# Kernel tuning notes

Measured on AMD Instinct MI355X. Metric: run time of the kernel, lower is better.

The kernel has to match this reference:

```python
import jax, jax.numpy as jnp
import numpy as np

TEMPERATURE = 5.0

def setup_inputs() -> dict:
    key = jax.random.key(0)
    k1, k2 = jax.random.split(key)
    B, D = 8192, 128
    features = jax.random.normal(k1, (B, D), dtype=jnp.float32)
    labels = jax.random.randint(k2, (B,), 0, 100, dtype=jnp.int64)
    return {"features": features, "labels": labels, "fac_label": 3}


def reference(features, labels, fac_label):
    # features: [B, D], labels: [B]
    B = features.shape[0]
    # positive-pair mask; note original's mask_scale row-copy loop is a no-op,
    # so mask_scale == mask, and mask_cross_feature == ones (fac_label unused in effect)
    mask = (labels[:, None] == labels[None, :]).astype(features.dtype)  # [B, B]

    sim = jnp.matmul(features, features.T) / TEMPERATURE  # [B, B]
    logits_max = jax.lax.stop_gradient(jnp.max(sim, axis=1, keepdims=True))
    logits = sim - logits_max

    # remove self-contrast (diagonal)
    logits_mask = 1.0 - jnp.eye(B, dtype=features.dtype)
    mask = mask * logits_mask

    exp_logits = jnp.exp(logits) * logits_mask
    log_prob = logits - jnp.log(1e-12 + exp_logits.sum(axis=1, keepdims=True))

    mean_log_prob_pos_mask = (mask * log_prob).sum(axis=1)  # [B]
    # vectorized form of the per-element reciprocal loop: 1/count where count>0 else 0
    cnt = mask.sum(axis=1)
    recip = jnp.where(cnt == 0, 0.0, 1.0 / jnp.where(cnt == 0, 1.0, cnt))

    loss = -(mean_log_prob_pos_mask * recip).mean()
    return loss
```

## Files before the change

### kernel.cpp

```cpp
#include <hip/hip_runtime.h>


#define BN 8192
#define DK 128
#define INV_T 0.2f
#define C1F 0.28853901f
#define C40F 27.7258872f

#define CHUNKS 32
#define CCOLS (BN / CHUNKS)
#define RPB 256
#define RT 4
#define NJT (CCOLS / 16)

#define NCLS 100
#define PB 128
#define PROWS (BN / PB)

#define OFF_FB    0
#define OFF_PART  (2 * 1024 * 1024)
#define OFF_GP    (OFF_PART + 2 * 1024 * 1024)
#define OFF_HISTP (OFF_GP + PB * NCLS * DK * 4)
#define OFF_G     (OFF_HISTP + PB * NCLS * 4)
#define OFF_HIST  (OFF_G + NCLS * DK * 4)
#define OFF_BSUM  (OFF_HIST + 512)
#define OFF_CTR   (OFF_BSUM + 256)

typedef __attribute__((ext_vector_type(8))) short bf16x8;
typedef __attribute__((ext_vector_type(4))) float f32x4;

__device__ __forceinline__ unsigned short f2bf(float f) {
    unsigned u = __builtin_bit_cast(unsigned, f);
    u += 0x7fffu + ((u >> 16) & 1u);
    return (unsigned short)(u >> 16);
}

__device__ __forceinline__ float fexp2(float x) {
#if __has_builtin(__builtin_amdgcn_exp2f)
    return __builtin_amdgcn_exp2f(x);
#else
    float r; asm("v_exp_f32 %0, %1" : "=v"(r) : "v"(x)); return r;
#endif
}

__device__ __forceinline__ void load_lds16(const void* g, void* l) {
    __builtin_amdgcn_global_load_lds(
        (const __attribute__((address_space(1))) unsigned int*)g,
        (__attribute__((address_space(3))) unsigned int*)l, 16, 0, 0);
}

__global__ __launch_bounds__(256) void prep_kernel(const float* __restrict__ F,
                                                   const int* __restrict__ labels,
                                                   unsigned short* __restrict__ Fb,
                                                   float* __restrict__ Gp,
                                                   int* __restrict__ histp,
                                                   unsigned int* __restrict__ ctr) {
    const int t  = threadIdx.x;
    const int b  = blockIdx.x;
    const int r0 = b * PROWS;

    if (b == 0 && t == 0) *ctr = 0u;

    const float4* F4  = (const float4*)F + (size_t)b * (PROWS * DK / 4);
    ushort4*      Fb4 = (ushort4*)Fb + (size_t)b * (PROWS * DK / 4);
#pragma unroll
    for (int k = 0; k < PROWS * DK / 4 / 256; ++k) {
        float4 v = F4[k * 256 + t];
        ushort4 o;
        o.x = f2bf(v.x); o.y = f2bf(v.y); o.z = f2bf(v.z); o.w = f2bf(v.w);
        Fb4[k * 256 + t] = o;
    }

    __shared__ int   lh[NCLS];
    __shared__ float gl[NCLS][DK];
    float* glf = (float*)gl;
    if (t < NCLS) lh[t] = 0;
#pragma unroll
    for (int k = 0; k < NCLS * DK / 256; ++k) glf[k * 256 + t] = 0.f;
    __syncthreads();

    if (t < PROWS) atomicAdd(&lh[labels[r0 + t]], 1);

    if (t < DK) {
        for (int rr = 0; rr < PROWS; ++rr) {
            const int row = r0 + rr;
            const int c   = labels[row];
            gl[c][t] += F[(size_t)row * DK + t];
        }
    }
    __syncthreads();

    if (t < NCLS) histp[b * NCLS + t] = lh[t];
#pragma unroll
    for (int k = 0; k < NCLS * DK / 256; ++k) {
        const int idx = k * 256 + t;
        Gp[(size_t)b * (NCLS * DK) + idx] = glf[idx];
    }
}

template <bool DIAGBLK>
__device__ __forceinline__ void supcon_rows(const short* __restrict__ Fb,
                                            float2* __restrict__ part,
                                            int bx, int by, char* smem) {
    const int t    = threadIdx.x;
    const int wave = t >> 6, lane = t & 63;
    const int quad = lane >> 4, l16 = lane & 15;
    const int rowBase = bx * RPB + wave * (RT * 16);
    const int colBase = by * CCOLS;

    bf16x8 a[RT][4];
#pragma unroll
    for (int rt = 0; rt < RT; ++rt)
#pragma unroll
        for (int kt = 0; kt < 4; ++kt)
            a[rt][kt] = *(const bf16x8*)(Fb + (size_t)(rowBase + rt * 16 + l16) * DK
                                            + kt * 32 + quad * 8);

    float mr[RT][4], Zs[RT][4];
#pragma unroll
    for (int rt = 0; rt < RT; ++rt)
#pragma unroll
        for (int r = 0; r < 4; ++r) { mr[rt][r] = -__builtin_inff(); Zs[rt][r] = 0.f; }

    const int  L    = wave * 1024 + lane * 16;
    const int  sw   = (L & ~255) | ((L & 255) ^ ((L >> 4) & 0x70));
    const char* tile0 = (const char*)(Fb + (size_t)colBase * DK);
    char*       dst0  = smem + wave * 1024;

    int roff[4];
#pragma unroll
    for (int kt = 0; kt < 4; ++kt)
        roff[kt] = l16 * 256 + ((kt * 64 + quad * 16) ^ ((l16 & 7) << 4));

    auto STAGE = [&](int bufoff, int jt) {
        load_lds16(tile0 + (size_t)jt * 4096 + sw, dst0 + bufoff);
    };

    auto COMPUTE = [&](int bufoff, int jt) {
        bf16x8 bb[4];
#pragma unroll
        for (int kt = 0; kt < 4; ++kt)
            bb[kt] = *(const bf16x8*)(smem + bufoff + roff[kt]);
        const int j0 = colBase + jt * 16;
#pragma unroll
        for (int rt = 0; rt < RT; ++rt) {
            f32x4 acc = {0.f, 0.f, 0.f, 0.f};
#pragma unroll
            for (int kt = 0; kt < 4; ++kt)
                acc = __builtin_amdgcn_mfma_f32_16x16x32_bf16(a[rt][kt], bb[kt], acc, 0, 0, 0);
#pragma unroll
            for (int r = 0; r < 4; ++r) {
                const float raw = acc[r];
                mr[rt][r] = fmaxf(mr[rt][r], raw);
                float e = fexp2(fmaf(raw, C1F, -40.0f));
                if (DIAGBLK) {
                    const int irow0 = rowBase + rt * 16 + quad * 4;
                    if (j0 + l16 == irow0 + r) e = 0.f;
                }
                Zs[rt][r] += e;
            }
        }
    };

    STAGE(0, 0);
    __syncthreads();
    for (int jt = 0; jt < NJT; jt += 2) {
        STAGE(4096, jt + 1);
        COMPUTE(0, jt);
        __syncthreads();
        if (jt + 2 < NJT) STAGE(0, jt + 2);
        COMPUTE(4096, jt + 1);
        __syncthreads();
    }

#pragma unroll
    for (int rt = 0; rt < RT; ++rt)
#pragma unroll
        for (int r = 0; r < 4; ++r) {
            float mm = mr[rt][r], zz = Zs[rt][r];
#pragma unroll
            for (int h = 1; h < 16; h <<= 1) {
                mm = fmaxf(mm, __shfl_xor(mm, h));
                zz += __shfl_xor(zz, h);
            }
            if (l16 == 0)
                part[(size_t)by * BN + rowBase + rt * 16 + quad * 4 + r] =
                    make_float2(mm, zz);
        }
}

__global__ __launch_bounds__(256) void supcon_main(const short* __restrict__ Fb,
                                                   float2* __restrict__ part,
                                                   const float* __restrict__ Gp,
                                                   const int* __restrict__ histp,
                                                   float* __restrict__ G,
                                                   int* __restrict__ hist) {
    __shared__ alignas(16) char smem[8192];
    if (blockIdx.y == CHUNKS) {
        const int base = blockIdx.x * 256 + threadIdx.x;
        for (int idx = base; idx < NCLS * DK + NCLS; idx += BN) {
            if (idx < NCLS * DK) {
                float s = 0.f;
#pragma unroll 8
                for (int p = 0; p < PB; ++p) s += Gp[(size_t)p * (NCLS * DK) + idx];
                G[idx] = s;
            } else {
                const int c = idx - NCLS * DK;
                int s = 0;
#pragma unroll 8
                for (int p = 0; p < PB; ++p) s += histp[p * NCLS + c];
                hist[c] = s;
            }
        }
        return;
    }
    if (blockIdx.x == blockIdx.y) supcon_rows<true >(Fb, part, blockIdx.x, blockIdx.y, smem);
    else                          supcon_rows<false>(Fb, part, blockIdx.x, blockIdx.y, smem);
}

__global__ __launch_bounds__(256) void supcon_finalize(const float* __restrict__ F,
                                                       const int* __restrict__ labels,
                                                       const float2* __restrict__ part,
                                                       const float* __restrict__ G,
                                                       const int* __restrict__ hist,
                                                       float* __restrict__ bsums,
                                                       unsigned int* __restrict__ ctr,
                                                       float* __restrict__ out) {
    const int t = threadIdx.x;
    const int i = blockIdx.x * 256 + t;

    float mraw = -__builtin_inff(), Zm = 0.f;
#pragma unroll 8
    for (int c = 0; c < CHUNKS; ++c) {
        const float2 p = part[(size_t)c * BN + i];
        mraw = fmaxf(mraw, p.x);
        Zm += p.y;
    }
    const int   lbl = labels[i];
    const float cnt = (float)(hist[lbl] - 1);

    const float4* fr = (const float4*)(F + (size_t)i * DK);
    const float4* gr = (const float4*)(G + lbl * DK);
    float dot = 0.f, nrm = 0.f;
#pragma unroll 8
    for (int k = 0; k < DK / 4; ++k) {
        const float4 av = fr[k], gv = gr[k];
        dot += av.x * gv.x + av.y * gv.y + av.z * gv.z + av.w * gv.w;
        nrm += av.x * av.x + av.y * av.y + av.z * av.z + av.w * av.w;
    }

    const float m = mraw * INV_T;
    const float A = (dot - nrm) * INV_T;
    float term = 0.f;
    if (cnt > 0.5f)
        term = (A - cnt * m) / cnt - __logf(1e-12f + Zm * __expf(C40F - m));

    float sum = term;
#pragma unroll
    for (int h = 1; h < 64; h <<= 1) sum += __shfl_xor(sum, h);
    __shared__ float ss[4];
    if ((t & 63) == 0) ss[t >> 6] = sum;
    __syncthreads();
    if (t == 0) {
        bsums[blockIdx.x] = ss[0] + ss[1] + ss[2] + ss[3];
        __threadfence();
        const unsigned old = atomicAdd(ctr, 1u);
        if (old == (BN / 256) - 1) {
            __threadfence();
            float tot = 0.f;
            const volatile float* vb = bsums;
            for (int c = 0; c < BN / 256; ++c) tot += vb[c];
            out[0] = -tot * (1.0f / BN);
        }
    }
}

extern "C" void kernel_launch(void* const* d_in, const int* in_sizes, int n_in,
                              void* d_out, int out_size, void* d_ws, size_t ws_size,
                              hipStream_t stream) {
    const float* F      = (const float*)d_in[0];
    const int*   labels = (const int*)d_in[1];
    float* out = (float*)d_out;
    char*  ws  = (char*)d_ws;

    unsigned short* Fb    = (unsigned short*)(ws + OFF_FB);
    float2*         part  = (float2*)(ws + OFF_PART);
    float*          Gp    = (float*)(ws + OFF_GP);
    int*            histp = (int*)(ws + OFF_HISTP);
    float*          G     = (float*)(ws + OFF_G);
    int*            hist  = (int*)(ws + OFF_HIST);
    float*          bsums = (float*)(ws + OFF_BSUM);
    unsigned int*   ctr   = (unsigned int*)(ws + OFF_CTR);

    prep_kernel<<<PB, 256, 0, stream>>>(F, labels, Fb, Gp, histp, ctr);
    supcon_main<<<dim3(BN / RPB, CHUNKS + 1), 256, 0, stream>>>((const short*)Fb, part,
                                                                Gp, histp, G, hist);
    supcon_finalize<<<BN / 256, 256, 0, stream>>>(F, labels, part, G, hist,
                                                  bsums, ctr, out);
}
```

Before: 116.7 us.

## Deepen LDS staging to a four-buffer pipeline and parallelize class-sum prep

The main supcon loop moves from a double buffer to a four-slot LDS ring. Three tiles are prefetched ahead, and explicit vmcnt waits plus raw s_barrier calls replace __syncthreads, so global-to-LDS loads can overlap more MFMA work. The prep kernel now caches labels in LDS and uses all 256 threads, with two half-row groups accumulating into separate class-sum buffers that are summed on output. In exchange, LDS use doubles in both kernels, which may reduce occupancy, and the hand-written waitcnt and barrier sequencing has to stay correct.

Result: slower. 121.9 us (+4.4%).

```diff
diff --git a/kernel.cpp b/kernel.cpp
--- a/kernel.cpp
+++ b/kernel.cpp
@@ -28,6 +28,8 @@
 
 typedef __attribute__((ext_vector_type(8))) short bf16x8;
 typedef __attribute__((ext_vector_type(4))) float f32x4;
+
+#define FENCE() asm volatile("" ::: "memory")
 
 __device__ __forceinline__ unsigned short f2bf(float f) {
     unsigned u = __builtin_bit_cast(unsigned, f);
@@ -71,30 +73,35 @@
         Fb4[k * 256 + t] = o;
     }
 
+    __shared__ int   ll[PROWS];
     __shared__ int   lh[NCLS];
-    __shared__ float gl[NCLS][DK];
-    float* glf = (float*)gl;
+    __shared__ float gl[2][NCLS][DK];
+    float4* gl4 = (float4*)gl;
     if (t < NCLS) lh[t] = 0;
-#pragma unroll
-    for (int k = 0; k < NCLS * DK / 256; ++k) glf[k * 256 + t] = 0.f;
+    if (t < PROWS) ll[t] = labels[r0 + t];
+#pragma unroll
+    for (int k = 0; k < 2 * NCLS * DK / 4 / 256; ++k)
+        gl4[k * 256 + t] = make_float4(0.f, 0.f, 0.f, 0.f);
     __syncthreads();
 
-    if (t < PROWS) atomicAdd(&lh[labels[r0 + t]], 1);
-
-    if (t < DK) {
-        for (int rr = 0; rr < PROWS; ++rr) {
-            const int row = r0 + rr;
-            const int c   = labels[row];
-            gl[c][t] += F[(size_t)row * DK + t];
+    if (t < PROWS) atomicAdd(&lh[ll[t]], 1);
+
+    {
+        const int half = t >> 7, col = t & 127;
+        const int rb   = half * (PROWS / 2);
+        for (int rr = 0; rr < PROWS / 2; ++rr) {
+            const int lr = rb + rr;
+            gl[half][ll[lr]][col] += F[(size_t)(r0 + lr) * DK + col];
         }
     }
     __syncthreads();
 
     if (t < NCLS) histp[b * NCLS + t] = lh[t];
+    const float* gl0 = (const float*)gl;
 #pragma unroll
     for (int k = 0; k < NCLS * DK / 256; ++k) {
         const int idx = k * 256 + t;
-        Gp[(size_t)b * (NCLS * DK) + idx] = glf[idx];
+        Gp[(size_t)b * (NCLS * DK) + idx] = gl0[idx] + gl0[NCLS * DK + idx];
     }
 }
 
@@ -132,15 +139,15 @@
     for (int kt = 0; kt < 4; ++kt)
         roff[kt] = l16 * 256 + ((kt * 64 + quad * 16) ^ ((l16 & 7) << 4));
 
-    auto STAGE = [&](int bufoff, int jt) {
-        load_lds16(tile0 + (size_t)jt * 4096 + sw, dst0 + bufoff);
+    auto STAGE = [&](int buf, int jt) {
+        load_lds16(tile0 + (size_t)jt * 4096 + sw, dst0 + buf * 4096);
     };
 
-    auto COMPUTE = [&](int bufoff, int jt) {
+    auto COMPUTE = [&](int buf, int jt) {
         bf16x8 bb[4];
 #pragma unroll
         for (int kt = 0; kt < 4; ++kt)
-            bb[kt] = *(const bf16x8*)(smem + bufoff + roff[kt]);
+            bb[kt] = *(const bf16x8*)(smem + buf * 4096 + roff[kt]);
         const int j0 = colBase + jt * 16;
 #pragma unroll
         for (int rt = 0; rt < RT; ++rt) {
@@ -162,16 +169,27 @@
         }
     };
 
-    STAGE(0, 0);
-    __syncthreads();
-    for (int jt = 0; jt < NJT; jt += 2) {
-        STAGE(4096, jt + 1);
-        COMPUTE(0, jt);
-        __syncthreads();
-        if (jt + 2 < NJT) STAGE(0, jt + 2);
-        COMPUTE(4096, jt + 1);
-        __syncthreads();
-    }
+    STAGE(0, 0); STAGE(1, 1); STAGE(2, 2);
+    int jt = 0;
+    for (; jt < NJT - 2; ++jt) {
+        asm volatile("s_waitcnt vmcnt(2)" ::: "memory");
+        __builtin_amdgcn_s_barrier();
+        FENCE();
+        COMPUTE(jt & 3, jt);
+        FENCE();
+        __builtin_amdgcn_s_barrier();
+        FENCE();
+        if (jt + 3 < NJT) STAGE((jt + 3) & 3, jt + 3);
+    }
+    asm volatile("s_waitcnt vmcnt(1)" ::: "memory");
+    __builtin_amdgcn_s_barrier();
+    FENCE();
+    COMPUTE(jt & 3, jt);
+    ++jt;
+    asm volatile("s_waitcnt vmcnt(0)" ::: "memory");
+    __builtin_amdgcn_s_barrier();
+    FENCE();
+    COMPUTE(jt & 3, jt);
 
 #pragma unroll
     for (int rt = 0; rt < RT; ++rt)
@@ -195,7 +213,7 @@
                                                    const int* __restrict__ histp,
                                                    float* __restrict__ G,
                                                    int* __restrict__ hist) {
-    __shared__ alignas(16) char smem[8192];
+    __shared__ alignas(16) char smem[16384];
     if (blockIdx.y == CHUNKS) {
         const int base = blockIdx.x * 256 + threadIdx.x;
         for (int idx = base; idx < NCLS * DK + NCLS; idx += BN) {
```
